# Kernel tuning notes

Hardware: AMD Instinct MI355X
Metric: run time of the kernel (lower is better)

Reference implementation:

```python
import jax, jax.numpy as jnp
import numpy as np
from jax import lax

A = -0.75  # torch bicubic kernel coefficient
VGG_MEAN = np.array([0.485, 0.456, 0.406], np.float32).reshape(1, 3, 1, 1)
VGG_STD = np.array([0.229, 0.224, 0.225], np.float32).reshape(1, 3, 1, 1)
SCALE = 2
EPS = 1e-12


def _cubic(d):
    d = jnp.abs(d)
    return jnp.where(d <= 1, ((A + 2) * d - (A + 3)) * d * d + 1,
                     jnp.where(d < 2, A * (((d - 5) * d + 8) * d - 4), 0.0))


def _interp_axis(x, axis, out):
    # 1D bicubic interpolation with align_corners=True along `axis` (2 or 3)
    n = x.shape[axis]
    scale = (n - 1) / (out - 1)
    coords = jnp.arange(out, dtype=jnp.float32) * scale
    i0f = jnp.floor(coords)
    t = coords - i0f
    i0 = i0f.astype(jnp.int32)
    idx = jnp.clip(jnp.stack([i0 - 1, i0, i0 + 1, i0 + 2]), 0, n - 1)  # [4,out]
    w = jnp.stack([_cubic(t + 1), _cubic(t), _cubic(t - 1), _cubic(t - 2)])  # [4,out]
    g = jnp.take(x, idx, axis=axis)  # inserts [4,out] at `axis`
    if axis == 2:  # g: [B,C,4,out,W]
        return (g * w[None, None, :, :, None]).sum(axis=2)
    else:          # g: [B,C,H,4,out]
        return (g * w).sum(axis=3)


def upsample_bicubic_ac(x, f):
    B, C, H, W = x.shape
    x = _interp_axis(x, 2, H * f)
    x = _interp_axis(x, 3, W * f)
    return x


def conv2d(x, w, b, pad):
    y = lax.conv_general_dilated(x, w, (1, 1), [(pad, pad), (pad, pad)],
                                 dimension_numbers=('NCHW', 'OIHW', 'NCHW'))
    return y + b[None, :, None, None]


def maxpool2(x):
    return lax.reduce_window(x, -jnp.inf, lax.max, (1, 1, 2, 2), (1, 1, 2, 2), 'VALID')


def avgpool(x, s):
    return lax.reduce_window(x, 0.0, lax.add, (1, 1, s, s), (1, 1, s, s), 'VALID') / float(s * s)


def sub_mean(x):
    return (x - VGG_MEAN) / VGG_STD


def patches3(x):
    # torch Unfold(k=3, s=1, 'same' via reflection pad): [B, C*9, H*W], channel-major ordering
    B, C, H, W = x.shape
    xp = jnp.pad(x, ((0, 0), (0, 0), (1, 1), (1, 1)), mode='reflect')
    cols = jnp.stack([xp[:, :, i:i + H, j:j + W] for i in range(3) for j in range(3)], axis=2)
    return cols.reshape(B, C * 9, H * W)


def feats(x, w1, b1, w2, b2, w3, b3, w4, b4, wm, bm):
    # VGG19 features[0:10] + 1x1 map conv + LeakyReLU(0.2)
    x = jax.nn.relu(conv2d(x, w1, b1, 1))
    x = jax.nn.relu(conv2d(x, w2, b2, 1))
    x = maxpool2(x)
    x = jax.nn.relu(conv2d(x, w3, b3, 1))
    x = jax.nn.relu(conv2d(x, w4, b4, 1))
    x = maxpool2(x)
    x = conv2d(x, wm, bm, 0)
    return jnp.where(x > 0, x, 0.2 * x)


def _forward(query, key, w1, b1, w2, b2, w3, b3, w4, b4, wm, bm):
    q = feats(upsample_bicubic_ac(sub_mean(query), SCALE), w1, b1, w2, b2, w3, b3, w4, b4, wm, bm)
    B, C, Hq, Wq = q.shape
    qp = patches3(q)  # [B, C*9, Lq]

    k = avgpool(key, SCALE)
    k = feats(upsample_bicubic_ac(sub_mean(k), SCALE), w1, b1, w2, b2, w3, b3, w4, b4, wm, bm)
    kp = patches3(k)  # [B, C*9, Lk]

    w = jnp.swapaxes(kp, 1, 2)  # [B, Lk, C*9]
    w = w / jnp.maximum(jnp.linalg.norm(w, axis=2, keepdims=True), EPS)
    qn = qp / jnp.maximum(jnp.linalg.norm(qp, axis=1, keepdims=True), EPS)

    y = jnp.einsum('blc,bcm->blm', w, qn)  # [B, Lk, Lq] cosine similarity
    relevance = jnp.max(y, axis=1).reshape(B, 1, Hq, Wq)
    hard_indices = jnp.argmax(y, axis=1)  # [B, Lq]
    return relevance, hard_indices


def setup_inputs() -> dict:
    key0 = jax.random.key(0)
    ks = jax.random.split(key0, 8)

    def rn(k, shape, s):
        return jax.random.normal(k, shape, jnp.float32) * s

    return {
        'query': rn(ks[0], (2, 3, 160, 160), 1.0),
        'key': rn(ks[1], (2, 3, 320, 320), 1.0),
        'w1': rn(ks[2], (64, 3, 3, 3), 0.1),
        'b1': jnp.zeros((64,), jnp.float32),
        'w2': rn(ks[3], (64, 64, 3, 3), 0.05),
        'b2': jnp.zeros((64,), jnp.float32),
        'w3': rn(ks[4], (128, 64, 3, 3), 0.05),
        'b3': jnp.zeros((128,), jnp.float32),
        'w4': rn(ks[5], (128, 128, 3, 3), 0.04),
        'b4': jnp.zeros((128,), jnp.float32),
        'wm': rn(ks[6], (16, 128, 1, 1), 0.08),
        'bm': jnp.zeros((16,), jnp.float32),
    }


def reference(query, key, w1, b1, w2, b2, w3, b3, w4, b4, wm, bm):
    return _forward(query, key, w1, b1, w2, b2, w3, b3, w4, b4, wm, bm)
```

## Files before the change

kernel.cpp:

```cpp
#include <hip/hip_runtime.h>
#include <math.h>


__constant__ float VGG_M32_[3] = {0.485f, 0.456f, 0.406f};
__constant__ float VGG_S32_[3] = {0.229f, 0.224f, 0.225f};

__device__ __forceinline__ float bf16_to_f32(unsigned short u) {
    return __uint_as_float(((unsigned int)u) << 16);
}

__global__ void detect_dtype(const unsigned short* __restrict__ q, int* __restrict__ flag) {
    int t = threadIdx.x;
    int c = 0;
    for (int i = t; i < 2048; i += 64) {
        float v = bf16_to_f32(q[i]);
        float a = fabsf(v);
        if (!(a <= 64.0f)) c++;
    }
    for (int off = 32; off > 0; off >>= 1) c += __shfl_down(c, off, 64);
    if (t == 0) flag[0] = (c >= 4) ? 1 : 0;
}

__global__ void convert_in(const void* __restrict__ src, float* __restrict__ dst,
                           int n, const int* __restrict__ flag) {
    int i = blockIdx.x * blockDim.x + threadIdx.x;
    if (i >= n) return;
    if (flag[0]) dst[i] = ((const float*)src)[i];
    else         dst[i] = bf16_to_f32(((const unsigned short*)src)[i]);
}

__global__ void conv_w_f64(const float* __restrict__ src, double* __restrict__ dst, int n) {
    int i = blockIdx.x * blockDim.x + threadIdx.x;
    if (i < n) dst[i] = (double)src[i];
}

__device__ __forceinline__ float cubicw_np(float d) {
    d = fabsf(d);
    if (d <= 1.0f) {
        float p = (float)(1.25 * (double)d);
        p = (float)((double)p - 2.25);
        p = (float)((double)p * (double)d);
        p = (float)((double)p * (double)d);
        return (float)((double)p + 1.0);
    } else if (d < 2.0f) {
        float p = (float)((double)d - 5.0);
        p = (float)((double)p * (double)d);
        p = (float)((double)p + 8.0);
        p = (float)((double)p * (double)d);
        p = (float)((double)p - 4.0);
        return (float)(-0.75 * (double)p);
    }
    return 0.0f;
}

__global__ void sub_mean_k(const float* __restrict__ in, float* __restrict__ out, int N) {
    const int total = 3 * N * N;
    int idx = blockIdx.x * blockDim.x + threadIdx.x;
    if (idx >= total) return;
    int c = idx / (N * N);
    float t1 = (float)((double)in[idx] - (double)VGG_M32_[c]);
    out[idx] = (float)((double)t1 / (double)VGG_S32_[c]);
}

__global__ void avgpool2_k(const float* __restrict__ in, float* __restrict__ out, int OH) {
    const int total = 3 * OH * OH;
    int idx = blockIdx.x * blockDim.x + threadIdx.x;
    if (idx >= total) return;
    int x = idx % OH, y = (idx / OH) % OH, c = idx / (OH * OH);
    const int IW = 2 * OH;
    const float* p = in + (size_t)c * IW * IW;
    double s = (double)p[(2 * y) * IW + 2 * x] + (double)p[(2 * y) * IW + 2 * x + 1]
             + (double)p[(2 * y + 1) * IW + 2 * x] + (double)p[(2 * y + 1) * IW + 2 * x + 1];
    float s32 = (float)s;
    out[idx] = (float)((double)s32 / 4.0);
}

__global__ void maxpool2_k(const float* __restrict__ in, float* __restrict__ out, int C, int OH) {
    const int total = C * OH * OH;
    int idx = blockIdx.x * blockDim.x + threadIdx.x;
    if (idx >= total) return;
    int x = idx % OH, y = (idx / OH) % OH, c = idx / (OH * OH);
    const int IW = 2 * OH;
    const float* p = in + (size_t)c * IW * IW;
    float a = p[(2 * y) * IW + 2 * x],     b = p[(2 * y) * IW + 2 * x + 1];
    float cc = p[(2 * y + 1) * IW + 2 * x], d = p[(2 * y + 1) * IW + 2 * x + 1];
    out[idx] = fmaxf(fmaxf(fmaxf(a, b), cc), d);
}

__global__ void upsample_k(const float* __restrict__ in, float* __restrict__ out, int N) {
    const int NO = 2 * N;
    const int total = 3 * NO * NO;
    int idx = blockIdx.x * blockDim.x + threadIdx.x;
    if (idx >= total) return;
    int ox = idx % NO, oy = (idx / NO) % NO, c = idx / (NO * NO);

    const double scale = (double)(N - 1) / (double)(NO - 1);
    float cy = (float)((double)oy * scale);
    float fy = floorf(cy);
    float ty = cy - fy;
    int   iy = (int)fy;
    float cx = (float)((double)ox * scale);
    float fx = floorf(cx);
    float tx = cx - fx;
    int   ix = (int)fx;

    float wy[4], wx[4];
    wy[0] = cubicw_np((float)((double)ty + 1.0));
    wy[1] = cubicw_np(ty);
    wy[2] = cubicw_np((float)((double)ty - 1.0));
    wy[3] = cubicw_np((float)((double)ty - 2.0));
    wx[0] = cubicw_np((float)((double)tx + 1.0));
    wx[1] = cubicw_np(tx);
    wx[2] = cubicw_np((float)((double)tx - 1.0));
    wx[3] = cubicw_np((float)((double)tx - 2.0));

    int ys[4], xs[4];
#pragma unroll
    for (int i = 0; i < 4; ++i) {
        int y = iy - 1 + i; ys[i] = y < 0 ? 0 : (y > N - 1 ? N - 1 : y);
        int x = ix - 1 + i; xs[i] = x < 0 ? 0 : (x > N - 1 ? N - 1 : x);
    }
    const float* p = in + (size_t)c * N * N;

    float col[4];
#pragma unroll
    for (int j = 0; j < 4; ++j) {
        float p0 = (float)((double)wy[0] * (double)p[ys[0] * N + xs[j]]);
        float p1 = (float)((double)wy[1] * (double)p[ys[1] * N + xs[j]]);
        float p2 = (float)((double)wy[2] * (double)p[ys[2] * N + xs[j]]);
        float p3 = (float)((double)wy[3] * (double)p[ys[3] * N + xs[j]]);
        col[j] = (float)((double)p0 + (double)p1 + (double)p2 + (double)p3);
    }
    float q0 = (float)((double)wx[0] * (double)col[0]);
    float q1 = (float)((double)wx[1] * (double)col[1]);
    float q2 = (float)((double)wx[2] * (double)col[2]);
    float q3 = (float)((double)wx[3] * (double)col[3]);
    out[idx] = (float)((double)q0 + (double)q1 + (double)q2 + (double)q3);
}

template <int CIN, int HW, int CI_T>
__global__ __launch_bounds__(256, 2) void conv3x3_relu4_k(
    const float* __restrict__ in, const double* __restrict__ wt,
    const float* __restrict__ bias, float* __restrict__ out) {
    __shared__ float  tile[CI_T][34][34];
    __shared__ double wlds[CI_T * 40];
    const int tx = threadIdx.x, ty = threadIdx.y;
    const int tid = ty * 16 + tx;
    const int cog = blockIdx.z;
    const int x0 = blockIdx.x * 32, y0 = blockIdx.y * 32;
    const bool interior = (x0 >= 1) && (x0 + 33 <= HW) && (y0 >= 1) && (y0 + 33 <= HW);

    double acc[4][2][2];
#pragma unroll
    for (int co = 0; co < 4; ++co) {
        acc[co][0][0] = 0.0; acc[co][0][1] = 0.0; acc[co][1][0] = 0.0; acc[co][1][1] = 0.0;
    }

    for (int cig = 0; cig < CIN; cig += CI_T) {
        __syncthreads();
        if (interior) {
            const float* base = in + (size_t)cig * HW * HW + (size_t)(y0 - 1) * HW + (x0 - 1);
            for (int i = tid; i < CI_T * 34 * 34; i += 256) {
                int ci = i / (34 * 34);
                int rem = i % (34 * 34);
                int r = rem / 34, c = rem % 34;
                tile[ci][r][c] = base[(size_t)ci * HW * HW + r * HW + c];
            }
        } else {
            for (int i = tid; i < CI_T * 34 * 34; i += 256) {
                int ci = i / (34 * 34);
                int rem = i % (34 * 34);
                int r = rem / 34, c = rem % 34;
                int gy = y0 - 1 + r, gx = x0 - 1 + c;
                float v = 0.f;
                if (gy >= 0 && gy < HW && gx >= 0 && gx < HW)
                    v = in[(size_t)(cig + ci) * HW * HW + gy * HW + gx];
                tile[ci][r][c] = v;
            }
        }
        for (int i = tid; i < CI_T * 36; i += 256) {
            int ci = i / 36, rem = i % 36;
            int co = rem / 9, k = rem % 9;
            wlds[ci * 40 + co * 10 + k] =
                wt[(((size_t)(cog * 4 + co)) * CIN + (cig + ci)) * 9 + k];
        }
        __syncthreads();
#pragma unroll
        for (int cii = 0; cii < CI_T; ++cii) {
            double rd[4][4];
#pragma unroll
            for (int i = 0; i < 4; ++i) {
                const float* rowp = &tile[cii][ty * 2 + i][tx * 2];
                float2 a = *(const float2*)(rowp);
                float2 bq = *(const float2*)(rowp + 2);
                rd[i][0] = (double)a.x;  rd[i][1] = (double)a.y;
                rd[i][2] = (double)bq.x; rd[i][3] = (double)bq.y;
            }
#pragma unroll
            for (int co = 0; co < 4; ++co) {
                const double* wp = &wlds[cii * 40 + co * 10];
                double2 wA = *(const double2*)(wp);
                double2 wB = *(const double2*)(wp + 2);
                double2 wC = *(const double2*)(wp + 4);
                double2 wD = *(const double2*)(wp + 6);
                double w0 = wA.x, w1 = wA.y, w2 = wB.x, w3 = wB.y, w4 = wC.x;
                double w5 = wC.y, w6 = wD.x, w7 = wD.y, w8 = wp[8];
#pragma unroll
                for (int dy = 0; dy < 2; ++dy)
#pragma unroll
                    for (int dx = 0; dx < 2; ++dx) {
                        acc[co][dy][dx] += w0 * rd[dy][dx]     + w1 * rd[dy][dx + 1]     + w2 * rd[dy][dx + 2]
                                         + w3 * rd[dy + 1][dx] + w4 * rd[dy + 1][dx + 1] + w5 * rd[dy + 1][dx + 2]
                                         + w6 * rd[dy + 2][dx] + w7 * rd[dy + 2][dx + 1] + w8 * rd[dy + 2][dx + 2];
                    }
            }
        }
    }
#pragma unroll
    for (int co = 0; co < 4; ++co) {
        double bv = (double)bias[cog * 4 + co];
        float* op = out + (size_t)(cog * 4 + co) * HW * HW;
#pragma unroll
        for (int dy = 0; dy < 2; ++dy)
#pragma unroll
            for (int dx = 0; dx < 2; ++dx) {
                int y = y0 + ty * 2 + dy, x = x0 + tx * 2 + dx;
                float c32 = (float)acc[co][dy][dx];
                float yb  = (float)((double)c32 + bv);
                op[(size_t)y * HW + x] = fmaxf(yb, 0.f);
            }
    }
}

__global__ void conv1x1_leaky_k(const float* __restrict__ in, const float* __restrict__ w,
                                const float* __restrict__ bias, float* __restrict__ out) {
    const int total = 16 * 6400;
    int idx = blockIdx.x * blockDim.x + threadIdx.x;
    if (idx >= total) return;
    int p = idx % 6400, co = idx / 6400;
    const float* ip = in + p;
    double acc = 0.0;
#pragma unroll
    for (int ci = 0; ci < 128; ++ci) acc += (double)w[co * 128 + ci] * (double)ip[(size_t)ci * 6400];
    float c32 = (float)acc;
    float t = (float)((double)c32 + (double)bias[co]);
    out[idx] = t > 0.f ? t : (float)(0.2 * (double)t);
}

__global__ void patches_norm_k(const float* __restrict__ f, float* __restrict__ outm) {
    int idx = blockIdx.x * blockDim.x + threadIdx.x;
    if (idx >= 6400) return;
    int y = idx / 80, x = idx % 80;
    float* op = outm + (size_t)idx * 144;
    double ss = 0.0;
#pragma unroll
    for (int c = 0; c < 16; ++c) {
#pragma unroll
        for (int dy = 0; dy < 3; ++dy) {
            int yy = y + dy - 1;
            yy = yy < 0 ? 1 : (yy > 79 ? 78 : yy);
#pragma unroll
            for (int dx = 0; dx < 3; ++dx) {
                int xx = x + dx - 1;
                xx = xx < 0 ? 1 : (xx > 79 ? 78 : xx);
                float v = f[c * 6400 + yy * 80 + xx];
                op[c * 9 + dy * 3 + dx] = v;
                ss += (double)v * (double)v;
            }
        }
    }
    float nrm = (float)sqrt(ss);
    nrm = fmaxf(nrm, 1e-12f);
    for (int d = 0; d < 144; ++d) op[d] = (float)((double)op[d] / (double)nrm);
}

#define TM 64
#define TL 64
#define NSEG 10
#define KT_PER 10
#define RST 17
__global__ __launch_bounds__(256, 2) void simmax_k(const float* __restrict__ QN,
                                                   const float* __restrict__ KN,
                                                   double* __restrict__ pv, int* __restrict__ pl,
                                                   double* __restrict__ tv, int* __restrict__ tlx) {
    __shared__ float Qs[TM * 148];
    __shared__ float Ks[TL * 148];
    double* redv = (double*)Qs;
    int*    redl = (int*)(Qs + 2176);
    double* tredv = (double*)Ks;
    int*    tredl = (int*)(Ks + 2176);
    const int t = threadIdx.x;
    const int mg = t & 15;
    const int lg = t >> 4;
    const int mbase = blockIdx.x * TM;
    const int ks = blockIdx.y;
    const float* Qb = QN + (size_t)mbase * 144;

    for (int i = t * 4; i < TM * 144; i += 256 * 4) {
        int row = i / 144, d = i % 144;
        float4 v = *(const float4*)(Qb + (size_t)row * 144 + d);
        *(float4*)(&Qs[row * 148 + d]) = v;
    }
    double bestv[4];
    int    bestl[4];
#pragma unroll
    for (int i = 0; i < 4; ++i) { bestv[i] = -1e30; bestl[i] = 0; }

    for (int kt = 0; kt < KT_PER; ++kt) {
        const int l0 = ks * 640 + kt * TL;
        __syncthreads();
        for (int i = t * 4; i < TL * 144; i += 256 * 4) {
            int row = i / 144, d = i % 144;
            float4 v = *(const float4*)(KN + (size_t)(l0 + row) * 144 + d);
            *(float4*)(&Ks[row * 148 + d]) = v;
        }
        __syncthreads();
        double acc[4][4] = {};
        for (int d = 0; d < 144; d += 4) {
            float4 qv[4], kv[4];
#pragma unroll
            for (int i = 0; i < 4; ++i) qv[i] = *(const float4*)(&Qs[(mg + i * 16) * 148 + d]);
#pragma unroll
            for (int j = 0; j < 4; ++j) kv[j] = *(const float4*)(&Ks[(lg + j * 16) * 148 + d]);
#pragma unroll
            for (int i = 0; i < 4; ++i)
#pragma unroll
                for (int j = 0; j < 4; ++j)
                    acc[i][j] += (double)qv[i].x * kv[j].x + (double)qv[i].y * kv[j].y +
                                 (double)qv[i].z * kv[j].z + (double)qv[i].w * kv[j].w;
        }
#pragma unroll
        for (int i = 0; i < 4; ++i)
#pragma unroll
            for (int j = 0; j < 4; ++j) {
                int l = l0 + lg + j * 16;
                if (acc[i][j] > bestv[i]) { bestv[i] = acc[i][j]; bestl[i] = l; }
            }
        __syncthreads();
#pragma unroll
        for (int i = 0; i < 4; ++i) {
            double tb = acc[i][0];
            int    tl_ = l0 + lg;
#pragma unroll
            for (int j = 1; j < 4; ++j)
                if (acc[i][j] > tb) { tb = acc[i][j]; tl_ = l0 + lg + j * 16; }
            tredv[(mg + i * 16) * RST + lg] = tb;
            tredl[(mg + i * 16) * RST + lg] = tl_;
        }
        __syncthreads();
        if (t < TM) {
            double bv2 = tredv[t * RST + 0];
            int    bl2 = tredl[t * RST + 0];
#pragma unroll
            for (int g = 1; g < 16; ++g)
                if (tredv[t * RST + g] > bv2) { bv2 = tredv[t * RST + g]; bl2 = tredl[t * RST + g]; }
            size_t q = (size_t)(mbase + t);
            tv[q * 100 + ks * KT_PER + kt]  = bv2;
            tlx[q * 100 + ks * KT_PER + kt] = bl2;
        }
    }
    __syncthreads();
#pragma unroll
    for (int i = 0; i < 4; ++i) {
        redv[(mg + i * 16) * RST + lg] = bestv[i];
        redl[(mg + i * 16) * RST + lg] = bestl[i];
    }
    __syncthreads();
    if (t < TM) {
        double bv = redv[t * RST + 0];
        int    bl = redl[t * RST + 0];
#pragma unroll
        for (int g = 1; g < 16; ++g) {
            double v = redv[t * RST + g];
            int    l = redl[t * RST + g];
            if (v > bv || (v == bv && l < bl)) { bv = v; bl = l; }
        }
        size_t o = (size_t)ks * 6400 + (mbase + t);
        pv[o] = bv;
        pl[o] = bl;
    }
}

__global__ void merge1_k(const double* __restrict__ pv, const int* __restrict__ pl,
                         double* __restrict__ MQ, int* __restrict__ IQ,
                         float* __restrict__ out, int b) {
    int idx = blockIdx.x * blockDim.x + threadIdx.x;
    if (idx >= 6400) return;
    double bv = pv[idx];
    int    bl = pl[idx];
    for (int s = 1; s < NSEG; ++s) {
        double v = pv[(size_t)s * 6400 + idx];
        int    l = pl[(size_t)s * 6400 + idx];
        if (v > bv || (v == bv && l < bl)) { bv = v; bl = l; }
    }
    MQ[idx] = bv;
    IQ[idx] = bl;
    out[b * 6400 + idx] = (float)bv;
}

__device__ __forceinline__ bool better_cand(double v1, int l1, double v2, int l2) {
    if (v1 != v2) return v1 > v2;
    int a1 = l1 / 1600, a2 = l2 / 1600;
    if (a1 != a2) return a1 < a2;
    int g1 = l1 & 15, g2 = l2 & 15;
    if (g1 != g2) return g1 < g2;
    return l1 < l2;
}

__global__ __launch_bounds__(64) void fixup_k(const float* __restrict__ QN,
                                              const float* __restrict__ KN,
                                              const double* __restrict__ tv,
                                              const int* __restrict__ tlx,
                                              const double* __restrict__ MQ,
                                              const int* __restrict__ IQ,
                                              float* __restrict__ out, int b) {
    const int q = blockIdx.x;
    const int lane = threadIdx.x;
    const int I = IQ[q];
    const int lo = I - 112, hi = I + 112;
    const double* tvp = tv + (size_t)q * 100;
    const int*    tlp = tlx + (size_t)q * 100;

    double bv = -1e30;
    int    bl = 0x3FFFFFFF;

    for (int s = lane; s < 100; s += 64) {
        const int tlo = s * 64, thi = tlo + 63;
        if (thi < lo || tlo > hi) {
            double v = tvp[s];
            int    l = tlp[s];
            if (better_cand(v, l, bv, bl)) { bv = v; bl = l; }
        }
    }

    const float* qp = QN + (size_t)q * 144;
    for (int s = 0; s < 100; ++s) {
        const int tlo = s * 64, thi = tlo + 63;
        const bool outside = (thi < lo || tlo > hi);
        const bool inside  = (tlo >= lo && thi <= hi);
        if (outside || inside) continue;
        const int l = tlo + lane;
        int dl = l - I; if (dl < 0) dl = -dl;
        if (dl > 112) {
            const float* kp = KN + (size_t)l * 144;
            double acc = 0.0;
            for (int d = 0; d < 144; d += 4) {
                float4 qv = *(const float4*)(qp + d);
                float4 kv = *(const float4*)(kp + d);
                acc += (double)qv.x * kv.x + (double)qv.y * kv.y +
                       (double)qv.z * kv.z + (double)qv.w * kv.w;
            }
            if (better_cand(acc, l, bv, bl)) { bv = acc; bl = l; }
        }
    }

    for (int off = 32; off > 0; off >>= 1) {
        double ov = __shfl_xor(bv, off, 64);
        int    ol = __shfl_xor(bl, off, 64);
        if (better_cand(ov, ol, bv, bl)) { bv = ov; bl = ol; }
    }

    if (lane == 0) {
        const int l = bl;
        double gap = MQ[q] - bv;
        int dd = l - I;
        int ad = dd < 0 ? -dd : dd;
        int final = I;
        if (gap < 1e-6) {
            bool band1 = (ad >= 4080 && ad <= 4208);
            bool band2 = (ad >= 128 && ad <= 320);
            if (band1 && l < I) final = l;
            if (band2 && l > I) final = l;
        }
        out[2 * 6400 + b * 6400 + q] = (float)final;
    }
}

extern "C" void kernel_launch(void* const* d_in, const int* in_sizes, int n_in,
                              void* d_out, int out_size, void* d_ws, size_t ws_size,
                              hipStream_t stream) {
    double* wd = (double*)d_ws;
    double* PVd = wd;
    double* MQd = wd + 64000;
    double* WD1 = wd + 70400;
    double* WD2 = WD1 + 1728;
    double* WD3 = WD2 + 36864;
    double* WD4 = WD3 + 73728;
    int*    PLi = (int*)(WD4 + 147456);
    int*    IQi = PLi + 64000;
    float*  ws  = (float*)(IQi + 6400 + 64);
    float* X   = ws + 0;
    float* Y   = ws + 6553600;
    float* FQ  = ws + 13107200;
    float* QN  = ws + 13209600;
    float* KN  = ws + 14131200;
    float* CQ  = ws + 15052800;
    float* CK  = CQ + 153600;
    float* CW1 = CK + 614400;
    float* CB1 = CW1 + 1728;
    float* CW2 = CB1 + 64;
    float* CB2 = CW2 + 36864;
    float* CW3 = CB2 + 64;
    float* CB3 = CW3 + 73728;
    float* CW4 = CB3 + 128;
    float* CB4 = CW4 + 147456;
    float* CWM = CB4 + 128;
    float* CBM = CWM + 2048;
    int*   FLG = (int*)(CBM + 16);
    float* SUB = X;
    float* AVG = X + 100000;
    double* TVd = (double*)X;
    int*    TLi = (int*)(X + 1280000);

    detect_dtype<<<1, 64, 0, stream>>>((const unsigned short*)d_in[0], FLG);
    float* dsts[12] = {CQ, CK, CW1, CB1, CW2, CB2, CW3, CB3, CW4, CB4, CWM, CBM};
    for (int i = 0; i < 12; ++i) {
        int n = in_sizes[i];
        convert_in<<<(n + 255) / 256, 256, 0, stream>>>(d_in[i], dsts[i], n, FLG);
    }
    conv_w_f64<<<(1728   + 255) / 256, 256, 0, stream>>>(CW1, WD1, 1728);
    conv_w_f64<<<(36864  + 255) / 256, 256, 0, stream>>>(CW2, WD2, 36864);
    conv_w_f64<<<(73728  + 255) / 256, 256, 0, stream>>>(CW3, WD3, 73728);
    conv_w_f64<<<(147456 + 255) / 256, 256, 0, stream>>>(CW4, WD4, 147456);

    const dim3 cb(16, 16);
    float* out = (float*)d_out;

    for (int b = 0; b < 2; ++b) {
        const float* qb = CQ + (size_t)b * 3 * 160 * 160;
        const float* kb = CK + (size_t)b * 3 * 320 * 320;

        sub_mean_k<<<300, 256, 0, stream>>>(qb, SUB, 160);
        upsample_k<<<1200, 256, 0, stream>>>(SUB, Y, 160);
        conv3x3_relu4_k<3, 320, 3><<<dim3(10, 10, 16), cb, 0, stream>>>(Y, WD1, CB1, X);
        conv3x3_relu4_k<64, 320, 8><<<dim3(10, 10, 16), cb, 0, stream>>>(X, WD2, CB2, Y);
        maxpool2_k<<<6400, 256, 0, stream>>>(Y, X, 64, 160);
        conv3x3_relu4_k<64, 160, 8><<<dim3(5, 5, 32), cb, 0, stream>>>(X, WD3, CB3, Y);
        conv3x3_relu4_k<128, 160, 8><<<dim3(5, 5, 32), cb, 0, stream>>>(Y, WD4, CB4, X);
        maxpool2_k<<<3200, 256, 0, stream>>>(X, Y, 128, 80);
        conv1x1_leaky_k<<<400, 256, 0, stream>>>(Y, CWM, CBM, FQ);
        patches_norm_k<<<100, 64, 0, stream>>>(FQ, QN);

        avgpool2_k<<<300, 256, 0, stream>>>(kb, AVG, 160);
        sub_mean_k<<<300, 256, 0, stream>>>(AVG, SUB, 160);
        upsample_k<<<1200, 256, 0, stream>>>(SUB, Y, 160);
        conv3x3_relu4_k<3, 320, 3><<<dim3(10, 10, 16), cb, 0, stream>>>(Y, WD1, CB1, X);
        conv3x3_relu4_k<64, 320, 8><<<dim3(10, 10, 16), cb, 0, stream>>>(X, WD2, CB2, Y);
        maxpool2_k<<<6400, 256, 0, stream>>>(Y, X, 64, 160);
        conv3x3_relu4_k<64, 160, 8><<<dim3(5, 5, 32), cb, 0, stream>>>(X, WD3, CB3, Y);
        conv3x3_relu4_k<128, 160, 8><<<dim3(5, 5, 32), cb, 0, stream>>>(Y, WD4, CB4, X);
        maxpool2_k<<<3200, 256, 0, stream>>>(X, Y, 128, 80);
        conv1x1_leaky_k<<<400, 256, 0, stream>>>(Y, CWM, CBM, FQ);
        patches_norm_k<<<100, 64, 0, stream>>>(FQ, KN);

        simmax_k<<<dim3(100, NSEG, 1), 256, 0, stream>>>(QN, KN, PVd, PLi, TVd, TLi);
        merge1_k<<<25, 256, 0, stream>>>(PVd, PLi, MQd, IQi, out, b);
        fixup_k<<<6400, 64, 0, stream>>>(QN, KN, TVd, TLi, MQd, IQi, out, b);
    }
}
```

Before: 4.492 ms.

## Prefetch next input-channel tile into registers during conv compute

The 3x3 conv kernel now loads the next input-channel chunk from global memory into a register staging array while the current chunk is being computed, then writes it to shared memory at the start of the next iteration. This is meant to hide global load latency behind the FP64 FMA work. The cost is more registers per thread (CI_T*34*34/256 floats), which under launch_bounds(256,2) may cause spills or lower occupancy.

```diff
diff --git a/kernel.cpp b/kernel.cpp
--- a/kernel.cpp
+++ b/kernel.cpp
@@ -142,6 +142,8 @@
 __global__ __launch_bounds__(256, 2) void conv3x3_relu4_k(
     const float* __restrict__ in, const double* __restrict__ wt,
     const float* __restrict__ bias, float* __restrict__ out) {
+    constexpr int NELEM = CI_T * 34 * 34;
+    constexpr int ELEMS = (NELEM + 255) / 256;
     __shared__ float  tile[CI_T][34][34];
     __shared__ double wlds[CI_T * 40];
     const int tx = threadIdx.x, ty = threadIdx.y;
@@ -150,32 +152,59 @@
     const int x0 = blockIdx.x * 32, y0 = blockIdx.y * 32;
     const bool interior = (x0 >= 1) && (x0 + 33 <= HW) && (y0 >= 1) && (y0 + 33 <= HW);
 
+    float rstage[ELEMS];
+
+    auto loadChunk = [&](int cig) {
+        if (interior) {
+            const float* base = in + (size_t)cig * HW * HW + (size_t)(y0 - 1) * HW + (x0 - 1);
+#pragma unroll
+            for (int j = 0; j < ELEMS; ++j) {
+                int i = tid + j * 256;
+                float v = 0.f;
+                if (i < NELEM) {
+                    int ci = i / (34 * 34);
+                    int rem = i % (34 * 34);
+                    int r = rem / 34, c = rem % 34;
+                    v = base[(size_t)ci * HW * HW + r * HW + c];
+                }
+                rstage[j] = v;
+            }
+        } else {
+#pragma unroll
+            for (int j = 0; j < ELEMS; ++j) {
+                int i = tid + j * 256;
+                float v = 0.f;
+                if (i < NELEM) {
+                    int ci = i / (34 * 34);
+                    int rem = i % (34 * 34);
+                    int r = rem / 34, c = rem % 34;
+                    int gy = y0 - 1 + r, gx = x0 - 1 + c;
+                    if (gy >= 0 && gy < HW && gx >= 0 && gx < HW)
+                        v = in[(size_t)(cig + ci) * HW * HW + gy * HW + gx];
+                }
+                rstage[j] = v;
+            }
+        }
+    };
+
     double acc[4][2][2];
 #pragma unroll
     for (int co = 0; co < 4; ++co) {
         acc[co][0][0] = 0.0; acc[co][0][1] = 0.0; acc[co][1][0] = 0.0; acc[co][1][1] = 0.0;
     }
 
+    loadChunk(0);
+
     for (int cig = 0; cig < CIN; cig += CI_T) {
         __syncthreads();
-        if (interior) {
-            const float* base = in + (size_t)cig * HW * HW + (size_t)(y0 - 1) * HW + (x0 - 1);
-            for (int i = tid; i < CI_T * 34 * 34; i += 256) {
+#pragma unroll
+        for (int j = 0; j < ELEMS; ++j) {
+            int i = tid + j * 256;
+            if (i < NELEM) {
                 int ci = i / (34 * 34);
                 int rem = i % (34 * 34);
                 int r = rem / 34, c = rem % 34;
-                tile[ci][r][c] = base[(size_t)ci * HW * HW + r * HW + c];
-            }
-        } else {
-            for (int i = tid; i < CI_T * 34 * 34; i += 256) {
-                int ci = i / (34 * 34);
-                int rem = i % (34 * 34);
-                int r = rem / 34, c = rem % 34;
-                int gy = y0 - 1 + r, gx = x0 - 1 + c;
-                float v = 0.f;
-                if (gy >= 0 && gy < HW && gx >= 0 && gx < HW)
-                    v = in[(size_t)(cig + ci) * HW * HW + gy * HW + gx];
-                tile[ci][r][c] = v;
+                tile[ci][r][c] = rstage[j];
             }
         }
         for (int i = tid; i < CI_T * 36; i += 256) {
@@ -185,6 +214,7 @@
                 wt[(((size_t)(cog * 4 + co)) * CIN + (cig + ci)) * 9 + k];
         }
         __syncthreads();
+        if (cig + CI_T < CIN) loadChunk(cig + CI_T);
 #pragma unroll
         for (int cii = 0; cii < CI_T; ++cii) {
             double rd[4][4];
```

After: 7.605 ms. 1.69x slower.
